# Performance work log

Hardware: AMD Instinct MI355X
Metric: run time of the kernel (lower is better)

## Reference

```python
import jax, jax.numpy as jnp
import numpy as np

N, E, B, T, F, H, O = 50000, 800000, 16, 4, 128, 128, 128
LEAKY = 0.2  # PyG GATConv negative_slope default


def setup_inputs() -> dict:
    key = jax.random.key(0)
    ks = jax.random.split(key, 12)
    s = 0.05
    return {
        "x": jax.random.normal(ks[0], (T, N, F), jnp.float32),
        "edge_index": jax.random.randint(ks[1], (2, E), 0, N, dtype=jnp.int32),
        "batch_idx": jnp.sort(jax.random.randint(ks[2], (N,), 0, B, dtype=jnp.int32)),
        "W1": jax.random.normal(ks[3], (F, H), jnp.float32) * s,
        "att_src1": jax.random.normal(ks[4], (H,), jnp.float32) * s,
        "att_dst1": jax.random.normal(ks[5], (H,), jnp.float32) * s,
        "b1": jnp.zeros((H,), jnp.float32),
        "W2": jax.random.normal(ks[6], (H, O), jnp.float32) * s,
        "att_src2": jax.random.normal(ks[7], (O,), jnp.float32) * s,
        "att_dst2": jax.random.normal(ks[8], (O,), jnp.float32) * s,
        "b2": jnp.zeros((O,), jnp.float32),
    }


def gat_layer(h, src, dst, W, a_src, a_dst, b):
    # PyG GATConv, heads=1, concat=False, self-loops already appended.
    h = h @ W                                  # [N, out]
    alpha_s = h @ a_src                        # [N]
    alpha_d = h @ a_dst                        # [N]
    e = alpha_s[src] + alpha_d[dst]            # [E']
    e = jnp.where(e > 0, e, LEAKY * e)         # leaky_relu
    # softmax over incoming edges of each destination node (every node has a self-loop)
    m = jax.ops.segment_max(e, dst, num_segments=N)
    ex = jnp.exp(e - m[dst])
    z = jax.ops.segment_sum(ex, dst, num_segments=N)
    alpha = ex / z[dst]                        # [E']
    out = jax.ops.segment_sum(alpha[:, None] * h[src], dst, num_segments=N)
    return out + b


def reference(x, edge_index, batch_idx, W1, att_src1, att_dst1, b1, W2, att_src2, att_dst2, b2):
    loops = jnp.arange(N, dtype=edge_index.dtype)
    src = jnp.concatenate([edge_index[0], loops])  # add_self_loops (PyG default)
    dst = jnp.concatenate([edge_index[1], loops])
    ones = jnp.ones((N, 1), jnp.float32)
    cnt = jax.ops.segment_sum(ones, batch_idx, num_segments=B)  # [B,1]

    def per_snapshot(xt):
        h = gat_layer(xt, src, dst, W1, att_src1, att_dst1, b1)
        h = jax.nn.relu(h)                     # inter-layer ReLU (dropout=0, eval)
        h = gat_layer(h, src, dst, W2, att_src2, att_dst2, b2)
        return jax.ops.segment_sum(h, batch_idx, num_segments=B) / cnt  # mean pool [B,O]

    reps = jax.vmap(per_snapshot)(x)           # [T, B, O]
    return jnp.transpose(reps, (1, 0, 2))      # [B, T, O]
```

## Files before the change

kernel.cpp:

```cpp
#include <hip/hip_runtime.h>
#include <hip/hip_bf16.h>

#define LEAKY 0.2f

typedef __attribute__((ext_vector_type(8))) short bf16x8;
typedef __attribute__((ext_vector_type(4))) float f32x4;
typedef __attribute__((ext_vector_type(2))) float f32x2;


__global__ __launch_bounds__(256) void k_init(int* cnt, int* bstart, int n, int nb) {
    int i = blockIdx.x * 256 + threadIdx.x;
    if (i < n) cnt[i] = 1;
    if (i < nb) bstart[i] = n;
}

__global__ __launch_bounds__(256) void k_count(const int* __restrict__ dst, int* cnt, int e) {
    int i = blockIdx.x * 256 + threadIdx.x;
    if (i < e) atomicAdd(&cnt[dst[i]], 1);
}

__device__ inline int block_incl_scan(int v, int* lds) {
    int lane = threadIdx.x & 63, wid = threadIdx.x >> 6;
    int s = v;
#pragma unroll
    for (int o = 1; o < 64; o <<= 1) { int t = __shfl_up(s, o); if (lane >= o) s += t; }
    if (lane == 63) lds[wid] = s;
    __syncthreads();
    int add = 0;
#pragma unroll
    for (int ww = 0; ww < 3; ++ww) if (ww < wid) add += lds[ww];
    return s + add;
}

__global__ __launch_bounds__(256) void k_scanA(const int* __restrict__ cnt, int* bsum, int n) {
    __shared__ int lds[4];
    int i = blockIdx.x * 256 + threadIdx.x;
    int v = (i < n) ? ((cnt[i] + 15) & ~15) : 0;
    int s = block_incl_scan(v, lds);
    if (threadIdx.x == 255) bsum[blockIdx.x] = s;
}

__global__ __launch_bounds__(256) void k_scanB(int* bsum, int* boff, int nb) {
    __shared__ int lds[4];
    int i = threadIdx.x;
    int v = (i < nb) ? bsum[i] : 0;
    int s = block_incl_scan(v, lds);
    if (i < nb) boff[i] = s - v;
}

__global__ __launch_bounds__(256) void k_scanC(const int* __restrict__ cnt, const int* __restrict__ boff,
                                               int* row_ptr, int n) {
    __shared__ int lds[4];
    int i = blockIdx.x * 256 + threadIdx.x;
    int v = (i < n) ? ((cnt[i] + 15) & ~15) : 0;
    int s = block_incl_scan(v, lds) + boff[blockIdx.x];
    if (i < n) row_ptr[i + 1] = s;
    if (i == 0) row_ptr[0] = 0;
}

__global__ __launch_bounds__(256) void k_selfloop(const int* __restrict__ row_ptr, int* csr, int* cursor, int n) {
    int i = blockIdx.x * 256 + threadIdx.x;
    if (i < n) { int p = row_ptr[i]; csr[p] = i; cursor[i] = p + 1; }
}

__global__ __launch_bounds__(256) void k_scatter(const int* __restrict__ src, const int* __restrict__ dst,
                                                 int* cursor, int* csr, int e) {
    int i = blockIdx.x * 256 + threadIdx.x;
    if (i < e) { int p = atomicAdd(&cursor[dst[i]], 1); csr[p] = src[i]; }
}

__global__ __launch_bounds__(256) void k_pad(const int* __restrict__ row_ptr, const int* __restrict__ cursor,
                                             int* csr, int n) {
    int i = blockIdx.x * 256 + threadIdx.x;
    if (i >= n) return;
    int p = cursor[i], e = row_ptr[i + 1];
    int v = i | 0x80000000;
    for (; p < e; ++p) csr[p] = v;
}

__global__ __launch_bounds__(256) void k_bbounds(const int* __restrict__ bidx, int* bstart, int n) {
    int i = blockIdx.x * 256 + threadIdx.x;
    if (i < n) {
        int b = bidx[i];
        if (i == 0 || bidx[i - 1] != b) atomicMin(&bstart[b], i);
    }
}

__global__ void k_bfix(int* bstart, int n, int nb) {
    bstart[nb] = n;
    for (int b = nb - 1; b >= 0; --b)
        if (bstart[b] == n) bstart[b] = bstart[b + 1];
}

__device__ inline unsigned short bf16r(float x) {
    unsigned int u = __float_as_uint(x);
    u += 0x7fffu + ((u >> 16) & 1u);
    return (unsigned short)(u >> 16);
}

__device__ inline unsigned int bfpair(float lo, float hi) {
    unsigned int ul = __float_as_uint(lo); ul += 0x7fffu + ((ul >> 16) & 1u);
    unsigned int uh = __float_as_uint(hi); uh += 0x7fffu + ((uh >> 16) & 1u);
    return (ul >> 16) | (uh & 0xffff0000u);
}

template <bool ABF16>
__global__ __launch_bounds__(256) void k_gemm_mfma(
    const void* __restrict__ Asrc, const float* __restrict__ W,
    const float* __restrict__ asrc, const float* __restrict__ adst,
    unsigned char* __restrict__ hq, float* __restrict__ vas, float* __restrict__ vad,
    int nrows)
{
    __shared__ unsigned short Wt[128 * 136];
    int tid = threadIdx.x;
    int lane = tid & 63, wv = tid >> 6;
    int row0 = blockIdx.x * 128;
    int c0 = lane & 15, g = lane >> 4;

    {
        int k = tid >> 1;
        int n0 = (tid & 1) * 64;
        const float4* wr = (const float4*)&W[k * 128 + n0];
#pragma unroll
        for (int i = 0; i < 16; ++i) {
            float4 v = wr[i];
            int n = n0 + i * 4;
            Wt[(n + 0) * 136 + k] = bf16r(v.x);
            Wt[(n + 1) * 136 + k] = bf16r(v.y);
            Wt[(n + 2) * 136 + k] = bf16r(v.z);
            Wt[(n + 3) * 136 + k] = bf16r(v.w);
        }
    }
    __syncthreads();

    f32x4 acc[2][8];
#pragma unroll
    for (int mi = 0; mi < 2; ++mi)
#pragma unroll
        for (int ni = 0; ni < 8; ++ni)
#pragma unroll
            for (int q = 0; q < 4; ++q) acc[mi][ni][q] = 0.f;

    int rA[2];
#pragma unroll
    for (int mi = 0; mi < 2; ++mi)
        rA[mi] = min(row0 + wv * 32 + mi * 16 + c0, nrows - 1);

#pragma unroll
    for (int ks = 0; ks < 4; ++ks) {
        int k0 = ks * 32;
        bf16x8 af[2];
#pragma unroll
        for (int mi = 0; mi < 2; ++mi) {
            if (ABF16) {
                af[mi] = *(const bf16x8*)((const unsigned short*)Asrc + (size_t)rA[mi] * 128 + k0 + g * 8);
            } else {
                const float4* ap = (const float4*)((const float*)Asrc + (size_t)rA[mi] * 128 + k0 + g * 8);
                float4 f0 = ap[0], f1 = ap[1];
                uint4 p = make_uint4(bfpair(f0.x, f0.y), bfpair(f0.z, f0.w),
                                     bfpair(f1.x, f1.y), bfpair(f1.z, f1.w));
                af[mi] = *(bf16x8*)&p;
            }
        }
        bf16x8 bfr[8];
#pragma unroll
        for (int ni = 0; ni < 8; ++ni)
            bfr[ni] = *(const bf16x8*)&Wt[(ni * 16 + c0) * 136 + k0 + g * 8];
#pragma unroll
        for (int mi = 0; mi < 2; ++mi)
#pragma unroll
            for (int ni = 0; ni < 8; ++ni)
                acc[mi][ni] = __builtin_amdgcn_mfma_f32_16x16x32_bf16(af[mi], bfr[ni], acc[mi][ni], 0, 0, 0);
    }

    float as_s[8], ad_s[8];
#pragma unroll
    for (int ni = 0; ni < 8; ++ni) {
        as_s[ni] = asrc[ni * 16 + c0];
        ad_s[ni] = adst[ni * 16 + c0];
    }
#pragma unroll
    for (int mi = 0; mi < 2; ++mi) {
#pragma unroll
        for (int reg = 0; reg < 4; ++reg) {
            int row = row0 + wv * 32 + mi * 16 + g * 4 + reg;
            bool rowok = row < nrows;
            float v[8];
            float s = 0.f, d = 0.f;
#pragma unroll
            for (int ni = 0; ni < 8; ++ni) {
                v[ni] = acc[mi][ni][reg];
                s = fmaf(v[ni], as_s[ni], s);
                d = fmaf(v[ni], ad_s[ni], d);
            }
#pragma unroll
            for (int o = 1; o < 16; o <<= 1) { s += __shfl_xor(s, o); d += __shfl_xor(d, o); }
            if (rowok && c0 == 0) { vas[row] = s; vad[row] = d; }
#pragma unroll
            for (int ni = 0; ni < 8; ++ni) {
                float vn = __shfl_xor(v[ni], 1);
                unsigned int w = (unsigned int)__builtin_amdgcn_cvt_pk_fp8_f32(v[ni], vn, 0, false);
                if (rowok && (c0 & 1) == 0)
                    *(unsigned short*)&hq[(size_t)row * 128 + ni * 16 + c0] = (unsigned short)w;
            }
        }
    }
}

template <bool RELU>
__global__ __launch_bounds__(256) void k_agg(const unsigned char* __restrict__ hq,
                                             const float* __restrict__ vas,
                                             const float* __restrict__ vad,
                                             const int* __restrict__ row_ptr,
                                             const int* __restrict__ csr,
                                             const float* __restrict__ bias,
                                             unsigned int* __restrict__ outb, int n) {
    int tid = threadIdx.x;
    int grp = tid >> 4, l = tid & 15;
    int w = blockIdx.x * 16 + grp;
    if (w >= n) return;
    unsigned int tbase = (unsigned int)blockIdx.y * (unsigned int)n;
    unsigned int g = tbase + (unsigned int)w;
    int beg = row_ptr[w], end = row_ptr[w + 1];
    float advl = vad[g];

    f32x2 acc2[4];
#pragma unroll
    for (int q = 0; q < 4; ++q) { acc2[q].x = 0.f; acc2[q].y = 0.f; }
    float zp = 0.f;

    for (int c = beg; c < end; c += 16) {
        int raw = csr[c + l];
        unsigned int s_l = tbase + (unsigned int)(raw & 0x7fffffff);
        float e = vas[s_l] + advl;
        e = e > 0.f ? e : LEAKY * e;
        float w_l = (raw >= 0) ? __expf(e) : 0.f;
        zp += w_l;

        unsigned int ofs[16]; float wt[16];
#pragma unroll
        for (int q = 0; q < 16; ++q) {
            ofs[q] = __shfl(s_l, q, 16) * 128u + (unsigned int)(l * 8);
            wt[q] = __shfl(w_l, q, 16);
        }
        uint2 v[16];
#pragma unroll
        for (int q = 0; q < 16; ++q)
            v[q] = *(const uint2*)&hq[ofs[q]];
#pragma unroll
        for (int q = 0; q < 16; ++q) {
            f32x2 w2; w2.x = wt[q]; w2.y = wt[q];
            acc2[0] = __builtin_elementwise_fma(w2, __builtin_amdgcn_cvt_pk_f32_fp8(v[q].x, false), acc2[0]);
            acc2[1] = __builtin_elementwise_fma(w2, __builtin_amdgcn_cvt_pk_f32_fp8(v[q].x, true),  acc2[1]);
            acc2[2] = __builtin_elementwise_fma(w2, __builtin_amdgcn_cvt_pk_f32_fp8(v[q].y, false), acc2[2]);
            acc2[3] = __builtin_elementwise_fma(w2, __builtin_amdgcn_cvt_pk_f32_fp8(v[q].y, true),  acc2[3]);
        }
    }

    float z = zp;
#pragma unroll
    for (int o = 1; o < 16; o <<= 1) z += __shfl_xor(z, o, 16);
    float inv = 1.0f / z;

    float4 b0 = *(const float4*)&bias[l * 8];
    float4 b1 = *(const float4*)&bias[l * 8 + 4];
    float4 o0 = make_float4(fmaf(acc2[0].x, inv, b0.x), fmaf(acc2[0].y, inv, b0.y),
                            fmaf(acc2[1].x, inv, b0.z), fmaf(acc2[1].y, inv, b0.w));
    float4 o1 = make_float4(fmaf(acc2[2].x, inv, b1.x), fmaf(acc2[2].y, inv, b1.y),
                            fmaf(acc2[3].x, inv, b1.z), fmaf(acc2[3].y, inv, b1.w));
    if (RELU) {
        o0.x = fmaxf(o0.x, 0.f); o0.y = fmaxf(o0.y, 0.f); o0.z = fmaxf(o0.z, 0.f); o0.w = fmaxf(o0.w, 0.f);
        o1.x = fmaxf(o1.x, 0.f); o1.y = fmaxf(o1.y, 0.f); o1.z = fmaxf(o1.z, 0.f); o1.w = fmaxf(o1.w, 0.f);
    }
    uint4 p = make_uint4(bfpair(o0.x, o0.y), bfpair(o0.z, o0.w),
                         bfpair(o1.x, o1.y), bfpair(o1.z, o1.w));
    *(uint4*)&outb[(size_t)g * 64 + l * 4] = p;
}

__global__ __launch_bounds__(128) void k_pool(const unsigned int* __restrict__ h,
                                              const int* __restrict__ bstart,
                                              float* __restrict__ out, int n, int T) {
    int b = blockIdx.x;
    int chunk = blockIdx.y;
    int t = blockIdx.z;
    int f = threadIdx.x;
    int s = bstart[b], e = bstart[b + 1];
    int cnt = e - s;
    if (cnt <= 0) return;
    int len = (cnt + 31) / 32;
    int cs = s + chunk * len;
    int ce = min(cs + len, e);
    if (cs >= ce) return;
    const unsigned int* ht = h + (size_t)t * n * 64;
    float acc = 0.f;
    for (int nidx = cs; nidx < ce; ++nidx) {
        unsigned int v = ht[(size_t)nidx * 64 + (f >> 1)];
        acc += __uint_as_float((f & 1) ? (v & 0xffff0000u) : (v << 16));
    }
    atomicAdd(&out[(size_t)(b * T + t) * 128 + f], acc / (float)cnt);
}


extern "C" void kernel_launch(void* const* d_in, const int* in_sizes, int n_in,
                              void* d_out, int out_size, void* d_ws, size_t ws_size,
                              hipStream_t stream) {
    const float* x    = (const float*)d_in[0];
    const int*   ei   = (const int*)d_in[1];
    const int*   bidx = (const int*)d_in[2];
    const float* W1   = (const float*)d_in[3];
    const float* as1  = (const float*)d_in[4];
    const float* ad1  = (const float*)d_in[5];
    const float* b1   = (const float*)d_in[6];
    const float* W2   = (const float*)d_in[7];
    const float* as2  = (const float*)d_in[8];
    const float* ad2  = (const float*)d_in[9];
    const float* b2   = (const float*)d_in[10];
    float* out = (float*)d_out;

    const int E = in_sizes[1] / 2;
    const int N = in_sizes[2];
    const int T = in_sizes[0] / (N * 128);
    const int B = out_size / (T * 128);
    const int* src = ei;
    const int* dst = ei + E;
    const int NT = N * T;

    char* wsp = (char*)d_ws;
    auto alloc = [&](size_t bytes) { void* p = wsp; wsp += (bytes + 255) / 256 * 256; return p; };
    unsigned char* hq    = (unsigned char*)alloc((size_t)NT * 128);
    unsigned int* hb2    = (unsigned int*)alloc((size_t)NT * 64 * 4);
    float* vas           = (float*)alloc((size_t)NT * 4);
    float* vad           = (float*)alloc((size_t)NT * 4);
    int* row_ptr         = (int*)alloc((size_t)(N + 1) * 4);
    int* cnt             = (int*)alloc((size_t)N * 4);
    int* csr             = (int*)alloc(((size_t)E + 16ull * N + 64) * 4);
    int* bstart          = (int*)alloc((size_t)(B + 2) * 4);
    int  nScanB          = (N + 255) / 256;
    int* bsum            = (int*)alloc((size_t)nScanB * 4);
    int* boff            = (int*)alloc((size_t)nScanB * 4);

    hipMemsetAsync(d_out, 0, (size_t)out_size * sizeof(float), stream);

    int gN = (N + 255) / 256, gE = (E + 255) / 256;
    k_init<<<gN, 256, 0, stream>>>(cnt, bstart, N, B + 1);
    k_count<<<gE, 256, 0, stream>>>(dst, cnt, E);
    k_scanA<<<nScanB, 256, 0, stream>>>(cnt, bsum, N);
    k_scanB<<<1, 256, 0, stream>>>(bsum, boff, nScanB);
    k_scanC<<<nScanB, 256, 0, stream>>>(cnt, boff, row_ptr, N);
    k_selfloop<<<gN, 256, 0, stream>>>(row_ptr, csr, cnt, N);
    k_scatter<<<gE, 256, 0, stream>>>(src, dst, cnt, csr, E);
    k_pad<<<gN, 256, 0, stream>>>(row_ptr, cnt, csr, N);
    k_bbounds<<<gN, 256, 0, stream>>>(bidx, bstart, N);
    k_bfix<<<1, 1, 0, stream>>>(bstart, N, B);

    int gGemm = (NT + 127) / 128;
    int gAgg = (N + 15) / 16;
    k_gemm_mfma<false><<<gGemm, 256, 0, stream>>>(x,   W1, as1, ad1, hq, vas, vad, NT);
    k_agg<true ><<<dim3(gAgg, T), 256, 0, stream>>>(hq, vas, vad, row_ptr, csr, b1, hb2, N);
    k_gemm_mfma<true ><<<gGemm, 256, 0, stream>>>(hb2, W2, as2, ad2, hq, vas, vad, NT);
    k_agg<false><<<dim3(gAgg, T), 256, 0, stream>>>(hq, vas, vad, row_ptr, csr, b2, hb2, N);
    k_pool<<<dim3(B, 32, T), 128, 0, stream>>>(hb2, bstart, out, N, T);
}
```

Measured before the change: 345.8 us.

## Fuse CSR setup kernels and interleave aggregation blocks across snapshots

The batch-boundary detection is folded into the edge count kernel, the boundary fixup into the single-block scan, and the self-loop insertion into the final scan pass. This removes three small launches. The aggregation grid becomes 1D, with block index decoded so that consecutive blocks cover the same node chunk across the four snapshots. Blocks that run at the same time then share row_ptr/csr reads in L2. The k_count change relies on gE being at least gN so every node gets checked, which holds here since E > N.

Measured after the change: 350.5 us. About the same (+1.3%).

```diff
diff --git a/kernel.cpp b/kernel.cpp
--- a/kernel.cpp
+++ b/kernel.cpp
@@ -14,9 +14,14 @@
     if (i < nb) bstart[i] = n;
 }
 
-__global__ __launch_bounds__(256) void k_count(const int* __restrict__ dst, int* cnt, int e) {
+__global__ __launch_bounds__(256) void k_count(const int* __restrict__ dst, int* cnt, int e,
+                                               const int* __restrict__ bidx, int* bstart, int n) {
     int i = blockIdx.x * 256 + threadIdx.x;
     if (i < e) atomicAdd(&cnt[dst[i]], 1);
+    if (i < n) {
+        int b = bidx[i];
+        if (i == 0 || bidx[i - 1] != b) atomicMin(&bstart[b], i);
+    }
 }
 
 __device__ inline int block_incl_scan(int v, int* lds) {
@@ -40,27 +45,33 @@
     if (threadIdx.x == 255) bsum[blockIdx.x] = s;
 }
 
-__global__ __launch_bounds__(256) void k_scanB(int* bsum, int* boff, int nb) {
+__global__ __launch_bounds__(256) void k_scanB(int* bsum, int* boff, int nb,
+                                               int* bstart, int n, int nbatch) {
     __shared__ int lds[4];
     int i = threadIdx.x;
     int v = (i < nb) ? bsum[i] : 0;
     int s = block_incl_scan(v, lds);
     if (i < nb) boff[i] = s - v;
+    if (i == 0) {
+        bstart[nbatch] = n;
+        for (int b = nbatch - 1; b >= 0; --b)
+            if (bstart[b] == n) bstart[b] = bstart[b + 1];
+    }
 }
 
 __global__ __launch_bounds__(256) void k_scanC(const int* __restrict__ cnt, const int* __restrict__ boff,
-                                               int* row_ptr, int n) {
+                                               int* row_ptr, int* csr, int* cursor, int n) {
     __shared__ int lds[4];
     int i = blockIdx.x * 256 + threadIdx.x;
     int v = (i < n) ? ((cnt[i] + 15) & ~15) : 0;
     int s = block_incl_scan(v, lds) + boff[blockIdx.x];
-    if (i < n) row_ptr[i + 1] = s;
+    if (i < n) {
+        int excl = s - v;
+        row_ptr[i + 1] = s;
+        csr[excl] = i;
+        cursor[i] = excl + 1;
+    }
     if (i == 0) row_ptr[0] = 0;
-}
-
-__global__ __launch_bounds__(256) void k_selfloop(const int* __restrict__ row_ptr, int* csr, int* cursor, int n) {
-    int i = blockIdx.x * 256 + threadIdx.x;
-    if (i < n) { int p = row_ptr[i]; csr[p] = i; cursor[i] = p + 1; }
 }
 
 __global__ __launch_bounds__(256) void k_scatter(const int* __restrict__ src, const int* __restrict__ dst,
@@ -76,20 +87,6 @@
     int p = cursor[i], e = row_ptr[i + 1];
     int v = i | 0x80000000;
     for (; p < e; ++p) csr[p] = v;
-}
-
-__global__ __launch_bounds__(256) void k_bbounds(const int* __restrict__ bidx, int* bstart, int n) {
-    int i = blockIdx.x * 256 + threadIdx.x;
-    if (i < n) {
-        int b = bidx[i];
-        if (i == 0 || bidx[i - 1] != b) atomicMin(&bstart[b], i);
-    }
-}
-
-__global__ void k_bfix(int* bstart, int n, int nb) {
-    bstart[nb] = n;
-    for (int b = nb - 1; b >= 0; --b)
-        if (bstart[b] == n) bstart[b] = bstart[b + 1];
 }
 
 __device__ inline unsigned short bf16r(float x) {
@@ -214,12 +211,18 @@
                                              const int* __restrict__ row_ptr,
                                              const int* __restrict__ csr,
                                              const float* __restrict__ bias,
-                                             unsigned int* __restrict__ outb, int n) {
+                                             unsigned int* __restrict__ outb,
+                                             int n, int chunksPerT) {
+    int i = blockIdx.x;
+    int slot = i & 7;
+    int t = slot >> 1;
+    int chunk = ((i >> 3) << 1) | (slot & 1);
+    if (chunk >= chunksPerT) return;
     int tid = threadIdx.x;
     int grp = tid >> 4, l = tid & 15;
-    int w = blockIdx.x * 16 + grp;
+    int w = chunk * 16 + grp;
     if (w >= n) return;
-    unsigned int tbase = (unsigned int)blockIdx.y * (unsigned int)n;
+    unsigned int tbase = (unsigned int)t * (unsigned int)n;
     unsigned int g = tbase + (unsigned int)w;
     int beg = row_ptr[w], end = row_ptr[w + 1];
     float advl = vad[g];
@@ -343,21 +346,20 @@
 
     int gN = (N + 255) / 256, gE = (E + 255) / 256;
     k_init<<<gN, 256, 0, stream>>>(cnt, bstart, N, B + 1);
-    k_count<<<gE, 256, 0, stream>>>(dst, cnt, E);
+    k_count<<<gE, 256, 0, stream>>>(dst, cnt, E, bidx, bstart, N);
     k_scanA<<<nScanB, 256, 0, stream>>>(cnt, bsum, N);
-    k_scanB<<<1, 256, 0, stream>>>(bsum, boff, nScanB);
-    k_scanC<<<nScanB, 256, 0, stream>>>(cnt, boff, row_ptr, N);
-    k_selfloop<<<gN, 256, 0, stream>>>(row_ptr, csr, cnt, N);
+    k_scanB<<<1, 256, 0, stream>>>(bsum, boff, nScanB, bstart, N, B);
+    k_scanC<<<nScanB, 256, 0, stream>>>(cnt, boff, row_ptr, csr, cnt, N);
     k_scatter<<<gE, 256, 0, stream>>>(src, dst, cnt, csr, E);
     k_pad<<<gN, 256, 0, stream>>>(row_ptr, cnt, csr, N);
-    k_bbounds<<<gN, 256, 0, stream>>>(bidx, bstart, N);
-    k_bfix<<<1, 1, 0, stream>>>(bstart, N, B);
 
     int gGemm = (NT + 127) / 128;
-    int gAgg = (N + 15) / 16;
+    int chunksPerT = (N + 15) / 16;
+    int chunksPad = ((chunksPerT + 1) / 2) * 2;
+    int gAggFlat = chunksPad * 4;
     k_gemm_mfma<false><<<gGemm, 256, 0, stream>>>(x,   W1, as1, ad1, hq, vas, vad, NT);
-    k_agg<true ><<<dim3(gAgg, T), 256, 0, stream>>>(hq, vas, vad, row_ptr, csr, b1, hb2, N);
+    k_agg<true ><<<gAggFlat, 256, 0, stream>>>(hq, vas, vad, row_ptr, csr, b1, hb2, N, chunksPerT);
     k_gemm_mfma<true ><<<gGemm, 256, 0, stream>>>(hb2, W2, as2, ad2, hq, vas, vad, NT);
-    k_agg<false><<<dim3(gAgg, T), 256, 0, stream>>>(hq, vas, vad, row_ptr, csr, b2, hb2, N);
+    k_agg<false><<<gAggFlat, 256, 0, stream>>>(hq, vas, vad, row_ptr, csr, b2, hb2, N, chunksPerT);
     k_pool<<<dim3(B, 32, T), 128, 0, stream>>>(hb2, bstart, out, N, T);
 }
```
